# Optimization experiments

Measured on AMD Instinct MI355X. Metric: run time of the kernel, lower is better.

Reference implementation:

```python
import jax, jax.numpy as jnp
import numpy as np

B, H0, W0, C = 16, 56, 56, 96
NH, WS, SS = 3, 7, 3
HID, NCL, TAU = 384, 128, 0.5
EPS = 1e-6

def layernorm(x, g, b):
    m = jnp.mean(x, -1, keepdims=True)
    v = jnp.mean((x - m) ** 2, -1, keepdims=True)
    return (x - m) * jax.lax.rsqrt(v + 1e-5) * g + b

def setup_inputs() -> dict:
    key = jax.random.key(0)
    ks = jax.random.split(key, 16)
    s = lambda d: 1.0 / np.sqrt(d)
    return {
        "x": jax.random.normal(ks[0], (B, H0 * W0, C), jnp.float32),
        "norm1_g": jnp.ones((C,)), "norm1_b": jnp.zeros((C,)),
        "qkv_w": jax.random.normal(ks[1], (3 * C, C)) * s(C),
        "qkv_b": jnp.zeros((3 * C,)),
        "proj_w": jax.random.normal(ks[2], (C, C)) * s(C),
        "proj_b": jnp.zeros((C,)),
        "norm2_g": jnp.ones((C,)), "norm2_b": jnp.zeros((C,)),
        "ffn_norm_g": jnp.ones((C,)), "ffn_norm_b": jnp.zeros((C,)),
        "pin_w": jax.random.normal(ks[3], (HID, C)) * s(C),
        "pin_b": jnp.zeros((HID,)),
        "tm_inc": jax.random.normal(ks[4], (NCL, 2 * HID)) * 0.5,
        "tm_out": jax.random.normal(ks[5], (NCL, C)) * s(NCL),
        "gate": jnp.float32(0.5),
        "H": H0, "W": W0,
    }

def window_attention(win, qkv_w, qkv_b, proj_w, proj_b):
    N, T, Cc = win.shape
    hd = Cc // NH
    qkv = win @ qkv_w.T + qkv_b                      # [N, T, 3C]
    qkv = qkv.reshape(N, T, 3, NH, hd).transpose(2, 0, 3, 1, 4)
    q, k, v = qkv[0], qkv[1], qkv[2]                 # [N, nh, T, hd]
    attn = jax.nn.softmax(jnp.einsum('nhqd,nhkd->nhqk', q, k) * (hd ** -0.5), axis=-1)
    out = jnp.einsum('nhqk,nhkd->nhqd', attn, v).transpose(0, 2, 1, 3).reshape(N, T, Cc)
    return out @ proj_w.T + proj_b

def tm_ffn(x, ffn_norm_g, ffn_norm_b, pin_w, pin_b, tm_inc, tm_out, gate):
    # x: [B, T, C]
    Bb, T, Cc = x.shape
    y = jax.nn.sigmoid(layernorm(x, ffn_norm_g, ffn_norm_b) @ pin_w.T + pin_b)  # [B,T,HID]
    flat = y.reshape(Bb * T, HID)
    lits = jnp.clip(jnp.concatenate([flat, 1.0 - flat], axis=-1), EPS, 1.0)     # [N, 2*HID]
    m = jax.nn.sigmoid(tm_inc)
    hard = (m > TAU).astype(m.dtype)
    m_ste = m + jax.lax.stop_gradient(hard - m)      # binary via STE
    # binary mask -> conjunction prod_k l_k^{m_jk} = exp(log(l) @ m^T)
    clauses = jnp.exp(jnp.log(lits) @ m_ste.T)       # [N, NCL]
    logits = (clauses @ tm_out).reshape(Bb, T, Cc)
    g = jax.nn.sigmoid(gate)
    return g * logits + (1.0 - g) * jax.nn.sigmoid(logits)

def reference(x, norm1_g, norm1_b, qkv_w, qkv_b, proj_w, proj_b,
              norm2_g, norm2_b, ffn_norm_g, ffn_norm_b,
              pin_w, pin_b, tm_inc, tm_out, gate, H, W):
    Bb, L, Cc = x.shape
    shortcut = x
    y = layernorm(x, norm1_g, norm1_b).reshape(Bb, H, W, Cc)
    pad_h = (WS - H % WS) % WS
    pad_w = (WS - W % WS) % WS
    if pad_h or pad_w:
        y = jnp.pad(y, ((0, 0), (0, pad_h), (0, pad_w), (0, 0)))
    Hp, Wp = y.shape[1], y.shape[2]
    if SS > 0:
        y = jnp.roll(y, shift=(-SS, -SS), axis=(1, 2))
    # window partition
    y = y.reshape(Bb, Hp // WS, WS, Wp // WS, WS, Cc).transpose(0, 1, 3, 2, 4, 5)
    win = y.reshape(-1, WS * WS, Cc)
    a = window_attention(win, qkv_w, qkv_b, proj_w, proj_b)
    a = a.reshape(Bb, Hp // WS, Wp // WS, WS, WS, Cc)
    if SS > 0:
        a = jnp.roll(a, shift=(SS, SS), axis=(3, 4))
    # window reverse
    a = a.transpose(0, 1, 3, 2, 4, 5).reshape(Bb, Hp, Wp, Cc)
    if pad_h or pad_w:
        a = a[:, :H, :W, :]
    a = a.reshape(Bb, H * W, Cc)
    x1 = shortcut + a
    x2 = x1 + tm_ffn(layernorm(x1, norm2_g, norm2_b),
                     ffn_norm_g, ffn_norm_b, pin_w, pin_b, tm_inc, tm_out, gate)
    return x2
```

## Files before the change

### kernel.cpp

```cpp
#include <hip/hip_runtime.h>

#define NB 16
#define NHH 56
#define NWW 56
#define NC 96
#define NL (NHH*NWW)
#define NTOK (NB*NL)
#define WSZ 7
#define NT 49
#define SSH 3
#define NWIN 1024
#define HDIM 32
#define HID_ 384
#define NCL_ 128
#define NLIT 768
#define EPS_ 1e-6f

typedef unsigned short u16;
typedef unsigned int   u32;
typedef __attribute__((ext_vector_type(8))) short short8;
typedef __attribute__((ext_vector_type(4))) float f32x4;

__device__ __forceinline__ float us2f(u16 u) {
  union { u32 u; float f; } x; x.u = ((u32)u) << 16; return x.f;
}
__device__ __forceinline__ u16 f2us(float f) {
  union { float f; u32 u; } x; x.f = f;
  u32 lsb = (x.u >> 16) & 1u;
  return (u16)((x.u + 0x7fffu + lsb) >> 16);
}
__device__ __forceinline__ float sigmoidf_(float x) { return 1.f / (1.f + __expf(-x)); }

__global__ __launch_bounds__(256) void k0_prep(const float* __restrict__ tm_inc,
                                               const float* __restrict__ pin_w,
                                               const float* __restrict__ tm_out,
                                               const float* __restrict__ qkv_w,
                                               const float* __restrict__ proj_w,
                                               u16* __restrict__ maskb,
                                               u16* __restrict__ pinwb,
                                               u16* __restrict__ tmoT,
                                               u16* __restrict__ qkvwb,
                                               u16* __restrict__ projwb) {
  int idx = blockIdx.x * 256 + threadIdx.x;
  if (idx < NCL_ * NLIT)
    maskb[idx] = (tm_inc[idx] > 0.f) ? (u16)0x3F80 : (u16)0;
  if (idx < HID_ * NC)
    pinwb[idx] = f2us(pin_w[idx]);
  if (idx < NC * NCL_) {
    int c = idx / NCL_, k = idx - c * NCL_;
    tmoT[idx] = f2us(tm_out[(size_t)k * NC + c]);
  }
  if (idx < 3 * NC * NC)
    qkvwb[idx] = f2us(qkv_w[idx]);
  if (idx < NC * NC)
    projwb[idx] = f2us(proj_w[idx]);
}

__global__ __launch_bounds__(256) void k2_attn(const float* __restrict__ x,
                                               const float* __restrict__ n1g,
                                               const float* __restrict__ n1b,
                                               const u16* __restrict__ qkvwb,
                                               const float* __restrict__ qkv_b,
                                               const u16* __restrict__ projwb,
                                               const float* __restrict__ proj_b,
                                               float* __restrict__ x1) {
  __shared__ __align__(16) u16 syb[64 * 104];
  __shared__ __align__(16) u16 sq [64 * 104];
  __shared__ __align__(16) u16 sk [64 * 104];
  __shared__ __align__(16) u16 svT[96 * 72];
  __shared__ __align__(16) u16 sp [4 * 16 * 72];
  const int tid  = threadIdx.x;
  const int wave = tid >> 6;
  const int lane = tid & 63;
  const int l16  = lane & 15;
  const int quad = lane >> 4;
  const int win  = blockIdx.x;
  const int t0   = wave * 16;
  const int bb = win >> 6, wl = win & 63;
  const int hbase = (wl >> 3) * WSZ, wbase = (wl & 7) * WSZ;

  {
    const int t = tid >> 2, s = tid & 3;
    if (t < NT) {
      int hp = hbase + t / WSZ, wp = wbase + t % WSZ;
      int h = hp + SSH; if (h >= NHH) h -= NHH;
      int w = wp + SSH; if (w >= NWW) w -= NWW;
      const float* xp = x + ((size_t)bb * NL + (size_t)h * NWW + w) * NC;
      float4 v[6];
      float sum = 0.f;
      #pragma unroll
      for (int k = 0; k < 6; ++k) {
        v[k] = *reinterpret_cast<const float4*>(xp + s * 4 + k * 16);
        sum += v[k].x + v[k].y + v[k].z + v[k].w;
      }
      sum += __shfl_xor(sum, 1); sum += __shfl_xor(sum, 2);
      float mean = sum * (1.f / 96.f);
      float ssq = 0.f;
      #pragma unroll
      for (int k = 0; k < 6; ++k) {
        float d0 = v[k].x - mean, d1 = v[k].y - mean;
        float d2 = v[k].z - mean, d3 = v[k].w - mean;
        ssq += d0 * d0 + d1 * d1 + d2 * d2 + d3 * d3;
      }
      ssq += __shfl_xor(ssq, 1); ssq += __shfl_xor(ssq, 2);
      float rstd = rsqrtf(ssq * (1.f / 96.f) + 1e-5f);
      #pragma unroll
      for (int k = 0; k < 6; ++k) {
        int c = s * 4 + k * 16;
        const float4 g4 = *reinterpret_cast<const float4*>(n1g + c);
        const float4 b4 = *reinterpret_cast<const float4*>(n1b + c);
        syb[t * 104 + c + 0] = f2us((v[k].x - mean) * rstd * g4.x + b4.x);
        syb[t * 104 + c + 1] = f2us((v[k].y - mean) * rstd * g4.y + b4.y);
        syb[t * 104 + c + 2] = f2us((v[k].z - mean) * rstd * g4.z + b4.z);
        syb[t * 104 + c + 3] = f2us((v[k].w - mean) * rstd * g4.w + b4.w);
      }
    } else {
      #pragma unroll
      for (int k = 0; k < 6; ++k) {
        int c = s * 4 + k * 16;
        syb[t * 104 + c + 0] = 0; syb[t * 104 + c + 1] = 0;
        syb[t * 104 + c + 2] = 0; syb[t * 104 + c + 3] = 0;
      }
    }
  }
  __syncthreads();

  {
    short8 afr[3];
    #pragma unroll
    for (int ks = 0; ks < 3; ++ks)
      afr[ks] = *reinterpret_cast<const short8*>(&syb[(t0 + l16) * 104 + quad * 8 + ks * 32]);
    short8 rb[4][3];
    #pragma unroll
    for (int p = 0; p < 4; ++p)
      #pragma unroll
      for (int ks = 0; ks < 3; ++ks)
        rb[p][ks] = *reinterpret_cast<const short8*>(
            qkvwb + (size_t)(p * 16 + l16) * NC + quad * 8 + ks * 32);
    #pragma unroll
    for (int nt = 0; nt < 18; ++nt) {
      const int n0 = nt * 16;
      const float bias = qkv_b[n0 + l16];
      short8 b0 = rb[nt & 3][0], b1 = rb[nt & 3][1], b2 = rb[nt & 3][2];
      if (nt + 4 < 18) {
        #pragma unroll
        for (int ks = 0; ks < 3; ++ks)
          rb[nt & 3][ks] = *reinterpret_cast<const short8*>(
              qkvwb + (size_t)((nt + 4) * 16 + l16) * NC + quad * 8 + ks * 32);
      }
      f32x4 acc = {0.f, 0.f, 0.f, 0.f};
      acc = __builtin_amdgcn_mfma_f32_16x16x32_bf16(afr[0], b0, acc, 0, 0, 0);
      acc = __builtin_amdgcn_mfma_f32_16x16x32_bf16(afr[1], b1, acc, 0, 0, 0);
      acc = __builtin_amdgcn_mfma_f32_16x16x32_bf16(afr[2], b2, acc, 0, 0, 0);
      const int part = nt / 6;
      const int oc = n0 - part * 96 + l16;
      if (part < 2) {
        u16* dst = (part == 0) ? sq : sk;
        #pragma unroll
        for (int r = 0; r < 4; ++r)
          dst[(t0 + quad * 4 + r) * 104 + oc] = f2us(acc[r] + bias);
      } else {
        #pragma unroll
        for (int r = 0; r < 4; ++r)
          svT[oc * 72 + (t0 + quad * 4 + r)] = f2us(acc[r] + bias);
      }
    }
  }
  __syncthreads();

  u16* spw = sp + wave * 16 * 72;
  const float sscale = 0.17677669529663687f;
  for (int h = 0; h < 3; ++h) {
    const int d0 = h * HDIM;
    short8 qf = *reinterpret_cast<const short8*>(&sq[(t0 + l16) * 104 + d0 + quad * 8]);
    f32x4 s[4];
    #pragma unroll
    for (int nt = 0; nt < 4; ++nt) {
      short8 kf = *reinterpret_cast<const short8*>(&sk[(nt * 16 + l16) * 104 + d0 + quad * 8]);
      f32x4 a = {0.f, 0.f, 0.f, 0.f};
      s[nt] = __builtin_amdgcn_mfma_f32_16x16x32_bf16(qf, kf, a, 0, 0, 0);
    }
    #pragma unroll
    for (int nt = 0; nt < 4; ++nt)
      #pragma unroll
      for (int r = 0; r < 4; ++r) s[nt][r] *= sscale;
    if (l16 >= 1) {
      #pragma unroll
      for (int r = 0; r < 4; ++r) s[3][r] = -1e30f;
    }
    #pragma unroll
    for (int r = 0; r < 4; ++r) {
      float m = fmaxf(fmaxf(s[0][r], s[1][r]), fmaxf(s[2][r], s[3][r]));
      #pragma unroll
      for (int off = 8; off > 0; off >>= 1) m = fmaxf(m, __shfl_xor(m, off, 16));
      float e0 = __expf(s[0][r] - m), e1 = __expf(s[1][r] - m);
      float e2 = __expf(s[2][r] - m), e3 = __expf(s[3][r] - m);
      float sum = e0 + e1 + e2 + e3;
      #pragma unroll
      for (int off = 8; off > 0; off >>= 1) sum += __shfl_xor(sum, off, 16);
      float inv = 1.f / sum;
      const int row = quad * 4 + r;
      spw[row * 72 +      l16] = f2us(e0 * inv);
      spw[row * 72 + 16 + l16] = f2us(e1 * inv);
      spw[row * 72 + 32 + l16] = f2us(e2 * inv);
      spw[row * 72 + 48 + l16] = f2us(e3 * inv);
    }
    short8 pa[2];
    pa[0] = *reinterpret_cast<const short8*>(&spw[l16 * 72 + quad * 8]);
    pa[1] = *reinterpret_cast<const short8*>(&spw[l16 * 72 + 32 + quad * 8]);
    #pragma unroll
    for (int nt = 0; nt < 2; ++nt) {
      const int c0 = d0 + nt * 16;
      f32x4 acc = {0.f, 0.f, 0.f, 0.f};
      #pragma unroll
      for (int ks = 0; ks < 2; ++ks) {
        short8 vb = *reinterpret_cast<const short8*>(&svT[(c0 + l16) * 72 + ks * 32 + quad * 8]);
        acc = __builtin_amdgcn_mfma_f32_16x16x32_bf16(pa[ks], vb, acc, 0, 0, 0);
      }
      #pragma unroll
      for (int r = 0; r < 4; ++r)
        syb[(t0 + quad * 4 + r) * 104 + c0 + l16] = f2us(acc[r]);
    }
  }

  {
    short8 aa[3];
    #pragma unroll
    for (int ks = 0; ks < 3; ++ks)
      aa[ks] = *reinterpret_cast<const short8*>(&syb[(t0 + l16) * 104 + quad * 8 + ks * 32]);

    size_t tokr[4]; bool tval[4];
    #pragma unroll
    for (int r = 0; r < 4; ++r) {
      const int t = t0 + quad * 4 + r;
      tval[r] = (t < NT);
      int rr = t / WSZ + SSH; if (rr >= WSZ) rr -= WSZ;
      int qq = t % WSZ + SSH; if (qq >= WSZ) qq -= WSZ;
      tokr[r] = (size_t)bb * NL + (size_t)(hbase + rr) * NWW + (wbase + qq);
    }
    float xv[6][4];
    #pragma unroll
    for (int nt = 0; nt < 6; ++nt)
      #pragma unroll
      for (int r = 0; r < 4; ++r)
        xv[nt][r] = tval[r] ? x[tokr[r] * NC + nt * 16 + l16] : 0.f;

    short8 pbr[2][3];
    #pragma unroll
    for (int ks = 0; ks < 3; ++ks)
      pbr[0][ks] = *reinterpret_cast<const short8*>(
          projwb + (size_t)l16 * NC + quad * 8 + ks * 32);
    #pragma unroll
    for (int nt = 0; nt < 6; ++nt) {
      const int n0 = nt * 16;
      const float pb = proj_b[n0 + l16];
      short8 b0 = pbr[nt & 1][0], b1 = pbr[nt & 1][1], b2 = pbr[nt & 1][2];
      if (nt + 1 < 6) {
        #pragma unroll
        for (int ks = 0; ks < 3; ++ks)
          pbr[(nt + 1) & 1][ks] = *reinterpret_cast<const short8*>(
              projwb + (size_t)((nt + 1) * 16 + l16) * NC + quad * 8 + ks * 32);
      }
      f32x4 acc = {0.f, 0.f, 0.f, 0.f};
      acc = __builtin_amdgcn_mfma_f32_16x16x32_bf16(aa[0], b0, acc, 0, 0, 0);
      acc = __builtin_amdgcn_mfma_f32_16x16x32_bf16(aa[1], b1, acc, 0, 0, 0);
      acc = __builtin_amdgcn_mfma_f32_16x16x32_bf16(aa[2], b2, acc, 0, 0, 0);
      #pragma unroll
      for (int r = 0; r < 4; ++r) {
        if (tval[r])
          x1[tokr[r] * NC + n0 + l16] = xv[nt][r] + acc[r] + pb;
      }
    }
  }
}

__global__ __launch_bounds__(512) void k4_ffn(const float* __restrict__ x1,
                                              const float* __restrict__ g2,
                                              const float* __restrict__ b2,
                                              const float* __restrict__ gf,
                                              const float* __restrict__ bf,
                                              const u16* __restrict__ pinwb,
                                              const float* __restrict__ pin_b,
                                              const u16* __restrict__ maskb,
                                              const u16* __restrict__ tmoT,
                                              const float* __restrict__ gate,
                                              float* __restrict__ out) {
  __shared__ __align__(16) u16 szb[32 * 104];
  __shared__ __align__(16) u16 lit[32 * 776];
  __shared__ __align__(16) u16 claT[32 * 136];
  __shared__ __align__(16) float sx1[32 * 100];
  const int tid  = threadIdx.x;
  const int wave = tid >> 6;
  const int lane = tid & 63;
  const int l16  = lane & 15;
  const int quad = lane >> 4;
  const size_t tok0 = (size_t)blockIdx.x * 32;

  {
    const int t = tid >> 4, s = tid & 15;
    const float* xp = x1 + (tok0 + t) * NC;
    float2 v[3];
    float sum = 0.f;
    #pragma unroll
    for (int k = 0; k < 3; ++k) {
      const int c = s * 2 + k * 32;
      v[k] = *reinterpret_cast<const float2*>(xp + c);
      sum += v[k].x + v[k].y;
      *reinterpret_cast<float2*>(&sx1[t * 100 + c]) = v[k];
    }
    #pragma unroll
    for (int off = 8; off > 0; off >>= 1) sum += __shfl_xor(sum, off, 16);
    const float mean = sum * (1.f / 96.f);
    float ssq = 0.f;
    #pragma unroll
    for (int k = 0; k < 3; ++k) {
      float d0 = v[k].x - mean, d1 = v[k].y - mean;
      ssq += d0 * d0 + d1 * d1;
    }
    #pragma unroll
    for (int off = 8; off > 0; off >>= 1) ssq += __shfl_xor(ssq, off, 16);
    const float rstd = rsqrtf(ssq * (1.f / 96.f) + 1e-5f);
    float tv[6];
    float sum2 = 0.f;
    #pragma unroll
    for (int k = 0; k < 3; ++k) {
      const int c = s * 2 + k * 32;
      const float2 gg = *reinterpret_cast<const float2*>(g2 + c);
      const float2 bb = *reinterpret_cast<const float2*>(b2 + c);
      tv[2 * k]     = (v[k].x - mean) * rstd * gg.x + bb.x;
      tv[2 * k + 1] = (v[k].y - mean) * rstd * gg.y + bb.y;
      sum2 += tv[2 * k] + tv[2 * k + 1];
    }
    #pragma unroll
    for (int off = 8; off > 0; off >>= 1) sum2 += __shfl_xor(sum2, off, 16);
    const float mean2 = sum2 * (1.f / 96.f);
    float ssq2 = 0.f;
    #pragma unroll
    for (int k = 0; k < 3; ++k) {
      float d0 = tv[2 * k] - mean2, d1 = tv[2 * k + 1] - mean2;
      ssq2 += d0 * d0 + d1 * d1;
    }
    #pragma unroll
    for (int off = 8; off > 0; off >>= 1) ssq2 += __shfl_xor(ssq2, off, 16);
    const float rstd2 = rsqrtf(ssq2 * (1.f / 96.f) + 1e-5f);
    #pragma unroll
    for (int k = 0; k < 3; ++k) {
      const int c = s * 2 + k * 32;
      const float2 gg = *reinterpret_cast<const float2*>(gf + c);
      const float2 bb = *reinterpret_cast<const float2*>(bf + c);
      u16 lo = f2us((tv[2 * k]     - mean2) * rstd2 * gg.x + bb.x);
      u16 hi = f2us((tv[2 * k + 1] - mean2) * rstd2 * gg.y + bb.y);
      *reinterpret_cast<u32*>(&szb[t * 104 + c]) = (u32)lo | ((u32)hi << 16);
    }
  }
  __syncthreads();

  const float gv = sigmoidf_(gate[0]);

  short8 a_pin[2][3];
  #pragma unroll
  for (int mt = 0; mt < 2; ++mt)
    #pragma unroll
    for (int ks = 0; ks < 3; ++ks)
      a_pin[mt][ks] = *reinterpret_cast<const short8*>(
          &szb[(mt * 16 + l16) * 104 + quad * 8 + ks * 32]);

  {
    float pbias[3];
    #pragma unroll
    for (int i = 0; i < 3; ++i) pbias[i] = pin_b[(wave * 3 + i) * 16 + l16];
    short8 pb[2][3];
    #pragma unroll
    for (int ks = 0; ks < 3; ++ks)
      pb[0][ks] = *reinterpret_cast<const short8*>(
          pinwb + (size_t)(wave * 3 * 16 + l16) * NC + quad * 8 + ks * 32);
    #pragma unroll
    for (int i = 0; i < 3; ++i) {
      short8 b0 = pb[i & 1][0], b1 = pb[i & 1][1], b2 = pb[i & 1][2];
      if (i + 1 < 3) {
        const int n1 = (wave * 3 + i + 1) * 16;
        #pragma unroll
        for (int ks = 0; ks < 3; ++ks)
          pb[(i + 1) & 1][ks] = *reinterpret_cast<const short8*>(
              pinwb + (size_t)(n1 + l16) * NC + quad * 8 + ks * 32);
      }
      f32x4 acc0 = {0.f, 0.f, 0.f, 0.f}, acc1 = {0.f, 0.f, 0.f, 0.f};
      acc0 = __builtin_amdgcn_mfma_f32_16x16x32_bf16(a_pin[0][0], b0, acc0, 0, 0, 0);
      acc1 = __builtin_amdgcn_mfma_f32_16x16x32_bf16(a_pin[1][0], b0, acc1, 0, 0, 0);
      acc0 = __builtin_amdgcn_mfma_f32_16x16x32_bf16(a_pin[0][1], b1, acc0, 0, 0, 0);
      acc1 = __builtin_amdgcn_mfma_f32_16x16x32_bf16(a_pin[1][1], b1, acc1, 0, 0, 0);
      acc0 = __builtin_amdgcn_mfma_f32_16x16x32_bf16(a_pin[0][2], b2, acc0, 0, 0, 0);
      acc1 = __builtin_amdgcn_mfma_f32_16x16x32_bf16(a_pin[1][2], b2, acc1, 0, 0, 0);
      const int o = (wave * 3 + i) * 16 + l16;
      const float pbv = pbias[i];
      #pragma unroll
      for (int r = 0; r < 4; ++r) {
        float y0 = sigmoidf_(acc0[r] + pbv);
        float y1 = sigmoidf_(acc1[r] + pbv);
        const int ta = quad * 4 + r, tb = 16 + quad * 4 + r;
        lit[ta * 776 + o]       = f2us(__logf(fmaxf(y0, EPS_)));
        lit[ta * 776 + 384 + o] = f2us(__logf(fmaxf(1.f - y0, EPS_)));
        lit[tb * 776 + o]       = f2us(__logf(fmaxf(y1, EPS_)));
        lit[tb * 776 + 384 + o] = f2us(__logf(fmaxf(1.f - y1, EPS_)));
      }
    }
  }
  __syncthreads();

  {
    const int ct = wave;
    const u16* bp0 = maskb + (size_t)(ct * 16 + l16) * NLIT + quad * 8;
    short8 rb0[4];
    #pragma unroll
    for (int p = 0; p < 4; ++p)
      rb0[p] = *reinterpret_cast<const short8*>(bp0 + p * 32);
    f32x4 c00 = {0.f, 0.f, 0.f, 0.f}, c10 = {0.f, 0.f, 0.f, 0.f};
    #pragma unroll
    for (int ks = 0; ks < 24; ++ks) {
      const int k0 = ks * 32 + quad * 8;
      short8 a0 = *reinterpret_cast<const short8*>(&lit[l16 * 776 + k0]);
      short8 a1 = *reinterpret_cast<const short8*>(&lit[(16 + l16) * 776 + k0]);
      short8 b0 = rb0[ks & 3];
      if (ks + 4 < 24)
        rb0[ks & 3] = *reinterpret_cast<const short8*>(bp0 + (ks + 4) * 32);
      c00 = __builtin_amdgcn_mfma_f32_16x16x32_bf16(a0, b0, c00, 0, 0, 0);
      c10 = __builtin_amdgcn_mfma_f32_16x16x32_bf16(a1, b0, c10, 0, 0, 0);
    }
    #pragma unroll
    for (int r = 0; r < 4; ++r) {
      const int ta = quad * 4 + r, tb = 16 + quad * 4 + r;
      claT[ta * 136 + ct * 16 + l16] = f2us(__expf(c00[r]));
      claT[tb * 136 + ct * 16 + l16] = f2us(__expf(c10[r]));
    }
  }
  __syncthreads();

  if (wave < 6) {
    const int nt = wave;
    f32x4 acc0 = {0.f, 0.f, 0.f, 0.f}, acc1 = {0.f, 0.f, 0.f, 0.f};
    #pragma unroll
    for (int ks = 0; ks < 4; ++ks) {
      const int k0 = ks * 32 + quad * 8;
      short8 a0 = *reinterpret_cast<const short8*>(&claT[l16 * 136 + k0]);
      short8 a1 = *reinterpret_cast<const short8*>(&claT[(16 + l16) * 136 + k0]);
      short8 b = *reinterpret_cast<const short8*>(
          tmoT + (size_t)(nt * 16 + l16) * NCL_ + k0);
      acc0 = __builtin_amdgcn_mfma_f32_16x16x32_bf16(a0, b, acc0, 0, 0, 0);
      acc1 = __builtin_amdgcn_mfma_f32_16x16x32_bf16(a1, b, acc1, 0, 0, 0);
    }
    const int c = nt * 16 + l16;
    #pragma unroll
    for (int r = 0; r < 4; ++r) {
      const int ta = quad * 4 + r, tb = 16 + quad * 4 + r;
      float lg0 = acc0[r], lg1 = acc1[r];
      out[(tok0 + ta) * NC + c] = sx1[ta * 100 + c] + gv * lg0 + (1.f - gv) * sigmoidf_(lg0);
      out[(tok0 + tb) * NC + c] = sx1[tb * 100 + c] + gv * lg1 + (1.f - gv) * sigmoidf_(lg1);
    }
  }
}

extern "C" void kernel_launch(void* const* d_in, const int* in_sizes, int n_in,
                              void* d_out, int out_size, void* d_ws, size_t ws_size,
                              hipStream_t stream) {
  (void)in_sizes; (void)n_in; (void)out_size; (void)ws_size;
  const float* x      = (const float*)d_in[0];
  const float* n1g    = (const float*)d_in[1];
  const float* n1b    = (const float*)d_in[2];
  const float* qkv_w  = (const float*)d_in[3];
  const float* qkv_b  = (const float*)d_in[4];
  const float* proj_w = (const float*)d_in[5];
  const float* proj_b = (const float*)d_in[6];
  const float* n2g    = (const float*)d_in[7];
  const float* n2b    = (const float*)d_in[8];
  const float* fng    = (const float*)d_in[9];
  const float* fnb    = (const float*)d_in[10];
  const float* pin_w  = (const float*)d_in[11];
  const float* pin_b  = (const float*)d_in[12];
  const float* tm_inc = (const float*)d_in[13];
  const float* tm_out = (const float*)d_in[14];
  const float* gate   = (const float*)d_in[15];

  float* x1 = (float*)d_ws;
  u16* maskb = (u16*)(x1 + (size_t)NTOK * NC);
  u16* pinwb = maskb + NCL_ * NLIT;
  u16* tmoT  = pinwb + HID_ * NC;
  u16* qkvwb = tmoT + NC * NCL_;
  u16* projwb= qkvwb + 3 * NC * NC;

  hipLaunchKernelGGL(k0_prep, dim3(384), dim3(256), 0, stream,
                     tm_inc, pin_w, tm_out, qkv_w, proj_w, maskb, pinwb, tmoT, qkvwb, projwb);
  hipLaunchKernelGGL(k2_attn, dim3(NWIN), dim3(256), 0, stream,
                     x, n1g, n1b, qkvwb, qkv_b, projwb, proj_b, x1);
  hipLaunchKernelGGL(k4_ffn, dim3(NTOK / 32), dim3(512), 0, stream,
                     x1, n2g, n2b, fng, fnb, pinwb, pin_b, maskb, tmoT, gate, (float*)d_out);
}
```

Before: 202.0 us.

## Split FFN clause stage into two token passes to shrink LDS footprint

```diff
diff --git a/kernel.cpp b/kernel.cpp
--- a/kernel.cpp
+++ b/kernel.cpp
@@ -15,6 +15,7 @@
 #define NCL_ 128
 #define NLIT 768
 #define EPS_ 1e-6f
+#define LOG_EPS -13.815510558f
 
 typedef unsigned short u16;
 typedef unsigned int   u32;
@@ -285,10 +286,10 @@
                                               const u16* __restrict__ tmoT,
                                               const float* __restrict__ gate,
                                               float* __restrict__ out) {
-  __shared__ __align__(16) u16 szb[32 * 104];
-  __shared__ __align__(16) u16 lit[32 * 776];
-  __shared__ __align__(16) u16 claT[32 * 136];
-  __shared__ __align__(16) float sx1[32 * 100];
+  __shared__ __align__(16) u16 lit[16 * 776];
+  __shared__ __align__(16) u16 su[32 * 136];
+  u16* szb  = su;
+  u16* claT = su;
   const int tid  = threadIdx.x;
   const int wave = tid >> 6;
   const int lane = tid & 63;
@@ -306,7 +307,6 @@
       const int c = s * 2 + k * 32;
       v[k] = *reinterpret_cast<const float2*>(xp + c);
       sum += v[k].x + v[k].y;
-      *reinterpret_cast<float2*>(&sx1[t * 100 + c]) = v[k];
     }
     #pragma unroll
     for (int off = 8; off > 0; off >>= 1) sum += __shfl_xor(sum, off, 16);
@@ -365,75 +365,71 @@
       a_pin[mt][ks] = *reinterpret_cast<const short8*>(
           &szb[(mt * 16 + l16) * 104 + quad * 8 + ks * 32]);
 
-  {
-    float pbias[3];
-    #pragma unroll
-    for (int i = 0; i < 3; ++i) pbias[i] = pin_b[(wave * 3 + i) * 16 + l16];
-    short8 pb[2][3];
-    #pragma unroll
-    for (int ks = 0; ks < 3; ++ks)
-      pb[0][ks] = *reinterpret_cast<const short8*>(
-          pinwb + (size_t)(wave * 3 * 16 + l16) * NC + quad * 8 + ks * 32);
-    #pragma unroll
-    for (int i = 0; i < 3; ++i) {
-      short8 b0 = pb[i & 1][0], b1 = pb[i & 1][1], b2 = pb[i & 1][2];
-      if (i + 1 < 3) {
-        const int n1 = (wave * 3 + i + 1) * 16;
+  float pbias[3];
+  #pragma unroll
+  for (int i = 0; i < 3; ++i) pbias[i] = pin_b[(wave * 3 + i) * 16 + l16];
+
+  #pragma unroll
+  for (int pass = 0; pass < 2; ++pass) {
+    {
+      short8 pb[2][3];
+      #pragma unroll
+      for (int ks = 0; ks < 3; ++ks)
+        pb[0][ks] = *reinterpret_cast<const short8*>(
+            pinwb + (size_t)(wave * 3 * 16 + l16) * NC + quad * 8 + ks * 32);
+      #pragma unroll
+      for (int i = 0; i < 3; ++i) {
+        short8 b0 = pb[i & 1][0], b1 = pb[i & 1][1], b2 = pb[i & 1][2];
+        if (i + 1 < 3) {
+          const int n1 = (wave * 3 + i + 1) * 16;
+          #pragma unroll
+          for (int ks = 0; ks < 3; ++ks)
+            pb[(i + 1) & 1][ks] = *reinterpret_cast<const short8*>(
+                pinwb + (size_t)(n1 + l16) * NC + quad * 8 + ks * 32);
+        }
+        f32x4 acc = {0.f, 0.f, 0.f, 0.f};
+        acc = __builtin_amdgcn_mfma_f32_16x16x32_bf16(a_pin[pass][0], b0, acc, 0, 0, 0);
+        acc = __builtin_amdgcn_mfma_f32_16x16x32_bf16(a_pin[pass][1], b1, acc, 0, 0, 0);
+        acc = __builtin_amdgcn_mfma_f32_16x16x32_bf16(a_pin[pass][2], b2, acc, 0, 0, 0);
+        const int o = (wave * 3 + i) * 16 + l16;
+        const float pbv = pbias[i];
         #pragma unroll
-        for (int ks = 0; ks < 3; ++ks)
-          pb[(i + 1) & 1][ks] = *reinterpret_cast<const short8*>(
-              pinwb + (size_t)(n1 + l16) * NC + quad * 8 + ks * 32);
-      }
-      f32x4 acc0 = {0.f, 0.f, 0.f, 0.f}, acc1 = {0.f, 0.f, 0.f, 0.f};
-      acc0 = __builtin_amdgcn_mfma_f32_16x16x32_bf16(a_pin[0][0], b0, acc0, 0, 0, 0);
-      acc1 = __builtin_amdgcn_mfma_f32_16x16x32_bf16(a_pin[1][0], b0, acc1, 0, 0, 0);
-      acc0 = __builtin_amdgcn_mfma_f32_16x16x32_bf16(a_pin[0][1], b1, acc0, 0, 0, 0);
-      acc1 = __builtin_amdgcn_mfma_f32_16x16x32_bf16(a_pin[1][1], b1, acc1, 0, 0, 0);
-      acc0 = __builtin_amdgcn_mfma_f32_16x16x32_bf16(a_pin[0][2], b2, acc0, 0, 0, 0);
-      acc1 = __builtin_amdgcn_mfma_f32_16x16x32_bf16(a_pin[1][2], b2, acc1, 0, 0, 0);
-      const int o = (wave * 3 + i) * 16 + l16;
-      const float pbv = pbias[i];
+        for (int r = 0; r < 4; ++r) {
+          const float a = acc[r] + pbv;
+          const float sp = fmaxf(a, 0.f) + __logf(1.f + __expf(-fabsf(a)));
+          const int t = quad * 4 + r;
+          lit[t * 776 + o]       = f2us(fmaxf(a - sp, LOG_EPS));
+          lit[t * 776 + 384 + o] = f2us(fmaxf(-sp, LOG_EPS));
+        }
+      }
+    }
+    __syncthreads();
+
+    {
+      const int ct = wave;
+      const u16* bp0 = maskb + (size_t)(ct * 16 + l16) * NLIT + quad * 8;
+      short8 rb0[4];
+      #pragma unroll
+      for (int p = 0; p < 4; ++p)
+        rb0[p] = *reinterpret_cast<const short8*>(bp0 + p * 32);
+      f32x4 c00 = {0.f, 0.f, 0.f, 0.f};
+      #pragma unroll
+      for (int ks = 0; ks < 24; ++ks) {
+        const int k0 = ks * 32 + quad * 8;
+        short8 a0 = *reinterpret_cast<const short8*>(&lit[l16 * 776 + k0]);
+        short8 b0 = rb0[ks & 3];
+        if (ks + 4 < 24)
+          rb0[ks & 3] = *reinterpret_cast<const short8*>(bp0 + (ks + 4) * 32);
+        c00 = __builtin_amdgcn_mfma_f32_16x16x32_bf16(a0, b0, c00, 0, 0, 0);
+      }
       #pragma unroll
       for (int r = 0; r < 4; ++r) {
-        float y0 = sigmoidf_(acc0[r] + pbv);
-        float y1 = sigmoidf_(acc1[r] + pbv);
-        const int ta = quad * 4 + r, tb = 16 + quad * 4 + r;
-        lit[ta * 776 + o]       = f2us(__logf(fmaxf(y0, EPS_)));
-        lit[ta * 776 + 384 + o] = f2us(__logf(fmaxf(1.f - y0, EPS_)));
-        lit[tb * 776 + o]       = f2us(__logf(fmaxf(y1, EPS_)));
-        lit[tb * 776 + 384 + o] = f2us(__logf(fmaxf(1.f - y1, EPS_)));
-      }
-    }
-  }
-  __syncthreads();
-
-  {
-    const int ct = wave;
-    const u16* bp0 = maskb + (size_t)(ct * 16 + l16) * NLIT + quad * 8;
-    short8 rb0[4];
-    #pragma unroll
-    for (int p = 0; p < 4; ++p)
-      rb0[p] = *reinterpret_cast<const short8*>(bp0 + p * 32);
-    f32x4 c00 = {0.f, 0.f, 0.f, 0.f}, c10 = {0.f, 0.f, 0.f, 0.f};
-    #pragma unroll
-    for (int ks = 0; ks < 24; ++ks) {
-      const int k0 = ks * 32 + quad * 8;
-      short8 a0 = *reinterpret_cast<const short8*>(&lit[l16 * 776 + k0]);
-      short8 a1 = *reinterpret_cast<const short8*>(&lit[(16 + l16) * 776 + k0]);
-      short8 b0 = rb0[ks & 3];
-      if (ks + 4 < 24)
-        rb0[ks & 3] = *reinterpret_cast<const short8*>(bp0 + (ks + 4) * 32);
-      c00 = __builtin_amdgcn_mfma_f32_16x16x32_bf16(a0, b0, c00, 0, 0, 0);
-      c10 = __builtin_amdgcn_mfma_f32_16x16x32_bf16(a1, b0, c10, 0, 0, 0);
-    }
-    #pragma unroll
-    for (int r = 0; r < 4; ++r) {
-      const int ta = quad * 4 + r, tb = 16 + quad * 4 + r;
-      claT[ta * 136 + ct * 16 + l16] = f2us(__expf(c00[r]));
-      claT[tb * 136 + ct * 16 + l16] = f2us(__expf(c10[r]));
-    }
-  }
-  __syncthreads();
+        const int t = pass * 16 + quad * 4 + r;
+        claT[t * 136 + ct * 16 + l16] = f2us(__expf(c00[r]));
+      }
+    }
+    __syncthreads();
+  }
 
   if (wave < 6) {
     const int nt = wave;
@@ -453,8 +449,10 @@
     for (int r = 0; r < 4; ++r) {
       const int ta = quad * 4 + r, tb = 16 + quad * 4 + r;
       float lg0 = acc0[r], lg1 = acc1[r];
-      out[(tok0 + ta) * NC + c] = sx1[ta * 100 + c] + gv * lg0 + (1.f - gv) * sigmoidf_(lg0);
-      out[(tok0 + tb) * NC + c] = sx1[tb * 100 + c] + gv * lg1 + (1.f - gv) * sigmoidf_(lg1);
+      out[(tok0 + ta) * NC + c] =
+          x1[(tok0 + ta) * NC + c] + gv * lg0 + (1.f - gv) * sigmoidf_(lg0);
+      out[(tok0 + tb) * NC + c] =
+          x1[(tok0 + tb) * NC + c] + gv * lg1 + (1.f - gv) * sigmoidf_(lg1);
     }
   }
 }
```

New measurement: 235.9 us. 1.17x slower.

## Interleave literal layout, compute log-sigmoid directly, and shrink FFN shared memory

Applied to the files above, without the earlier changes.

```diff
diff --git a/kernel.cpp b/kernel.cpp
--- a/kernel.cpp
+++ b/kernel.cpp
@@ -15,6 +15,7 @@
 #define NCL_ 128
 #define NLIT 768
 #define EPS_ 1e-6f
+#define LOG_EPS -13.815510558f
 
 typedef unsigned short u16;
 typedef unsigned int   u32;
@@ -42,8 +43,12 @@
                                                u16* __restrict__ qkvwb,
                                                u16* __restrict__ projwb) {
   int idx = blockIdx.x * 256 + threadIdx.x;
-  if (idx < NCL_ * NLIT)
-    maskb[idx] = (tm_inc[idx] > 0.f) ? (u16)0x3F80 : (u16)0;
+  if (idx < NCL_ * NLIT) {
+    int k = idx / NLIT, j = idx - k * NLIT;
+    int o   = (j < HID_) ? j : (j - HID_);
+    int pos = (j < HID_) ? (2 * o) : (2 * o + 1);
+    maskb[(size_t)k * NLIT + pos] = (tm_inc[idx] > 0.f) ? (u16)0x3F80 : (u16)0;
+  }
   if (idx < HID_ * NC)
     pinwb[idx] = f2us(pin_w[idx]);
   if (idx < NC * NCL_) {
@@ -285,10 +290,10 @@
                                               const u16* __restrict__ tmoT,
                                               const float* __restrict__ gate,
                                               float* __restrict__ out) {
-  __shared__ __align__(16) u16 szb[32 * 104];
-  __shared__ __align__(16) u16 lit[32 * 776];
-  __shared__ __align__(16) u16 claT[32 * 136];
-  __shared__ __align__(16) float sx1[32 * 100];
+  __shared__ __align__(16) u16 lit[32 * 778];
+  __shared__ __align__(16) u16 su[32 * 140];
+  u16* szb  = su;
+  u16* claT = su;
   const int tid  = threadIdx.x;
   const int wave = tid >> 6;
   const int lane = tid & 63;
@@ -306,7 +311,6 @@
       const int c = s * 2 + k * 32;
       v[k] = *reinterpret_cast<const float2*>(xp + c);
       sum += v[k].x + v[k].y;
-      *reinterpret_cast<float2*>(&sx1[t * 100 + c]) = v[k];
     }
     #pragma unroll
     for (int off = 8; off > 0; off >>= 1) sum += __shfl_xor(sum, off, 16);
@@ -391,17 +395,21 @@
       acc1 = __builtin_amdgcn_mfma_f32_16x16x32_bf16(a_pin[1][1], b1, acc1, 0, 0, 0);
       acc0 = __builtin_amdgcn_mfma_f32_16x16x32_bf16(a_pin[0][2], b2, acc0, 0, 0, 0);
       acc1 = __builtin_amdgcn_mfma_f32_16x16x32_bf16(a_pin[1][2], b2, acc1, 0, 0, 0);
-      const int o = (wave * 3 + i) * 16 + l16;
+      const int o2 = ((wave * 3 + i) * 16 + l16) * 2;
       const float pbv = pbias[i];
       #pragma unroll
       for (int r = 0; r < 4; ++r) {
-        float y0 = sigmoidf_(acc0[r] + pbv);
-        float y1 = sigmoidf_(acc1[r] + pbv);
+        const float a0 = acc0[r] + pbv;
+        const float sp0 = fmaxf(a0, 0.f) + __logf(1.f + __expf(-fabsf(a0)));
+        const u16 la0 = f2us(fmaxf(a0 - sp0, LOG_EPS));
+        const u16 lb0 = f2us(fmaxf(-sp0, LOG_EPS));
+        const float a1 = acc1[r] + pbv;
+        const float sp1 = fmaxf(a1, 0.f) + __logf(1.f + __expf(-fabsf(a1)));
+        const u16 la1 = f2us(fmaxf(a1 - sp1, LOG_EPS));
+        const u16 lb1 = f2us(fmaxf(-sp1, LOG_EPS));
         const int ta = quad * 4 + r, tb = 16 + quad * 4 + r;
-        lit[ta * 776 + o]       = f2us(__logf(fmaxf(y0, EPS_)));
-        lit[ta * 776 + 384 + o] = f2us(__logf(fmaxf(1.f - y0, EPS_)));
-        lit[tb * 776 + o]       = f2us(__logf(fmaxf(y1, EPS_)));
-        lit[tb * 776 + 384 + o] = f2us(__logf(fmaxf(1.f - y1, EPS_)));
+        *reinterpret_cast<u32*>(&lit[ta * 778 + o2]) = (u32)la0 | ((u32)lb0 << 16);
+        *reinterpret_cast<u32*>(&lit[tb * 778 + o2]) = (u32)la1 | ((u32)lb1 << 16);
       }
     }
   }
@@ -418,8 +426,8 @@
     #pragma unroll
     for (int ks = 0; ks < 24; ++ks) {
       const int k0 = ks * 32 + quad * 8;
-      short8 a0 = *reinterpret_cast<const short8*>(&lit[l16 * 776 + k0]);
-      short8 a1 = *reinterpret_cast<const short8*>(&lit[(16 + l16) * 776 + k0]);
+      short8 a0 = *reinterpret_cast<const short8*>(&lit[l16 * 778 + k0]);
+      short8 a1 = *reinterpret_cast<const short8*>(&lit[(16 + l16) * 778 + k0]);
       short8 b0 = rb0[ks & 3];
       if (ks + 4 < 24)
         rb0[ks & 3] = *reinterpret_cast<const short8*>(bp0 + (ks + 4) * 32);
@@ -429,8 +437,8 @@
     #pragma unroll
     for (int r = 0; r < 4; ++r) {
       const int ta = quad * 4 + r, tb = 16 + quad * 4 + r;
-      claT[ta * 136 + ct * 16 + l16] = f2us(__expf(c00[r]));
-      claT[tb * 136 + ct * 16 + l16] = f2us(__expf(c10[r]));
+      claT[ta * 140 + ct * 16 + l16] = f2us(__expf(c00[r]));
+      claT[tb * 140 + ct * 16 + l16] = f2us(__expf(c10[r]));
     }
   }
   __syncthreads();
@@ -441,8 +449,8 @@
     #pragma unroll
     for (int ks = 0; ks < 4; ++ks) {
       const int k0 = ks * 32 + quad * 8;
-      short8 a0 = *reinterpret_cast<const short8*>(&claT[l16 * 136 + k0]);
-      short8 a1 = *reinterpret_cast<const short8*>(&claT[(16 + l16) * 136 + k0]);
+      short8 a0 = *reinterpret_cast<const short8*>(&claT[l16 * 140 + k0]);
+      short8 a1 = *reinterpret_cast<const short8*>(&claT[(16 + l16) * 140 + k0]);
       short8 b = *reinterpret_cast<const short8*>(
           tmoT + (size_t)(nt * 16 + l16) * NCL_ + k0);
       acc0 = __builtin_amdgcn_mfma_f32_16x16x32_bf16(a0, b, acc0, 0, 0, 0);
@@ -453,8 +461,10 @@
     for (int r = 0; r < 4; ++r) {
       const int ta = quad * 4 + r, tb = 16 + quad * 4 + r;
       float lg0 = acc0[r], lg1 = acc1[r];
-      out[(tok0 + ta) * NC + c] = sx1[ta * 100 + c] + gv * lg0 + (1.f - gv) * sigmoidf_(lg0);
-      out[(tok0 + tb) * NC + c] = sx1[tb * 100 + c] + gv * lg1 + (1.f - gv) * sigmoidf_(lg1);
+      out[(tok0 + ta) * NC + c] =
+          x1[(tok0 + ta) * NC + c] + gv * lg0 + (1.f - gv) * sigmoidf_(lg0);
+      out[(tok0 + tb) * NC + c] =
+          x1[(tok0 + tb) * NC + c] + gv * lg1 + (1.f - gv) * sigmoidf_(lg1);
     }
   }
 }
```

After: 204.8 us. No clear change (+1.4%).

## Shrink FFN kernel LDS by aliasing buffers and computing log-sigmoid directly

Applied to the files above, without the earlier changes.

```diff
diff --git a/kernel.cpp b/kernel.cpp
--- a/kernel.cpp
+++ b/kernel.cpp
@@ -15,6 +15,7 @@
 #define NCL_ 128
 #define NLIT 768
 #define EPS_ 1e-6f
+#define LOG_EPS -13.815510558f
 
 typedef unsigned short u16;
 typedef unsigned int   u32;
@@ -285,10 +286,10 @@
                                               const u16* __restrict__ tmoT,
                                               const float* __restrict__ gate,
                                               float* __restrict__ out) {
-  __shared__ __align__(16) u16 szb[32 * 104];
   __shared__ __align__(16) u16 lit[32 * 776];
-  __shared__ __align__(16) u16 claT[32 * 136];
-  __shared__ __align__(16) float sx1[32 * 100];
+  __shared__ __align__(16) u16 su[32 * 136];
+  u16* szb  = su;
+  u16* claT = su;
   const int tid  = threadIdx.x;
   const int wave = tid >> 6;
   const int lane = tid & 63;
@@ -306,7 +307,6 @@
       const int c = s * 2 + k * 32;
       v[k] = *reinterpret_cast<const float2*>(xp + c);
       sum += v[k].x + v[k].y;
-      *reinterpret_cast<float2*>(&sx1[t * 100 + c]) = v[k];
     }
     #pragma unroll
     for (int off = 8; off > 0; off >>= 1) sum += __shfl_xor(sum, off, 16);
@@ -369,50 +369,56 @@
     float pbias[3];
     #pragma unroll
     for (int i = 0; i < 3; ++i) pbias[i] = pin_b[(wave * 3 + i) * 16 + l16];
-    short8 pb[2][3];
-    #pragma unroll
-    for (int ks = 0; ks < 3; ++ks)
-      pb[0][ks] = *reinterpret_cast<const short8*>(
-          pinwb + (size_t)(wave * 3 * 16 + l16) * NC + quad * 8 + ks * 32);
+    short8 pb[3][3];
+    #pragma unroll
+    for (int i = 0; i < 3; ++i)
+      #pragma unroll
+      for (int ks = 0; ks < 3; ++ks)
+        pb[i][ks] = *reinterpret_cast<const short8*>(
+            pinwb + (size_t)((wave * 3 + i) * 16 + l16) * NC + quad * 8 + ks * 32);
     #pragma unroll
     for (int i = 0; i < 3; ++i) {
-      short8 b0 = pb[i & 1][0], b1 = pb[i & 1][1], b2 = pb[i & 1][2];
-      if (i + 1 < 3) {
-        const int n1 = (wave * 3 + i + 1) * 16;
-        #pragma unroll
-        for (int ks = 0; ks < 3; ++ks)
-          pb[(i + 1) & 1][ks] = *reinterpret_cast<const short8*>(
-              pinwb + (size_t)(n1 + l16) * NC + quad * 8 + ks * 32);
-      }
       f32x4 acc0 = {0.f, 0.f, 0.f, 0.f}, acc1 = {0.f, 0.f, 0.f, 0.f};
-      acc0 = __builtin_amdgcn_mfma_f32_16x16x32_bf16(a_pin[0][0], b0, acc0, 0, 0, 0);
-      acc1 = __builtin_amdgcn_mfma_f32_16x16x32_bf16(a_pin[1][0], b0, acc1, 0, 0, 0);
-      acc0 = __builtin_amdgcn_mfma_f32_16x16x32_bf16(a_pin[0][1], b1, acc0, 0, 0, 0);
-      acc1 = __builtin_amdgcn_mfma_f32_16x16x32_bf16(a_pin[1][1], b1, acc1, 0, 0, 0);
-      acc0 = __builtin_amdgcn_mfma_f32_16x16x32_bf16(a_pin[0][2], b2, acc0, 0, 0, 0);
-      acc1 = __builtin_amdgcn_mfma_f32_16x16x32_bf16(a_pin[1][2], b2, acc1, 0, 0, 0);
+      acc0 = __builtin_amdgcn_mfma_f32_16x16x32_bf16(a_pin[0][0], pb[i][0], acc0, 0, 0, 0);
+      acc1 = __builtin_amdgcn_mfma_f32_16x16x32_bf16(a_pin[1][0], pb[i][0], acc1, 0, 0, 0);
+      acc0 = __builtin_amdgcn_mfma_f32_16x16x32_bf16(a_pin[0][1], pb[i][1], acc0, 0, 0, 0);
+      acc1 = __builtin_amdgcn_mfma_f32_16x16x32_bf16(a_pin[1][1], pb[i][1], acc1, 0, 0, 0);
+      acc0 = __builtin_amdgcn_mfma_f32_16x16x32_bf16(a_pin[0][2], pb[i][2], acc0, 0, 0, 0);
+      acc1 = __builtin_amdgcn_mfma_f32_16x16x32_bf16(a_pin[1][2], pb[i][2], acc1, 0, 0, 0);
       const int o = (wave * 3 + i) * 16 + l16;
       const float pbv = pbias[i];
       #pragma unroll
       for (int r = 0; r < 4; ++r) {
-        float y0 = sigmoidf_(acc0[r] + pbv);
-        float y1 = sigmoidf_(acc1[r] + pbv);
+        const float a0 = acc0[r] + pbv;
+        const float sp0 = fmaxf(a0, 0.f) + __logf(1.f + __expf(-fabsf(a0)));
+        const float a1 = acc1[r] + pbv;
+        const float sp1 = fmaxf(a1, 0.f) + __logf(1.f + __expf(-fabsf(a1)));
         const int ta = quad * 4 + r, tb = 16 + quad * 4 + r;
-        lit[ta * 776 + o]       = f2us(__logf(fmaxf(y0, EPS_)));
-        lit[ta * 776 + 384 + o] = f2us(__logf(fmaxf(1.f - y0, EPS_)));
-        lit[tb * 776 + o]       = f2us(__logf(fmaxf(y1, EPS_)));
-        lit[tb * 776 + 384 + o] = f2us(__logf(fmaxf(1.f - y1, EPS_)));
+        lit[ta * 776 + o]       = f2us(fmaxf(a0 - sp0, LOG_EPS));
+        lit[ta * 776 + 384 + o] = f2us(fmaxf(-sp0, LOG_EPS));
+        lit[tb * 776 + o]       = f2us(fmaxf(a1 - sp1, LOG_EPS));
+        lit[tb * 776 + 384 + o] = f2us(fmaxf(-sp1, LOG_EPS));
       }
     }
   }
   __syncthreads();
+
+  float xr[2][4];
+  if (wave < 6) {
+    const int c = wave * 16 + l16;
+    #pragma unroll
+    for (int r = 0; r < 4; ++r) {
+      xr[0][r] = x1[(tok0 + quad * 4 + r) * NC + c];
+      xr[1][r] = x1[(tok0 + 16 + quad * 4 + r) * NC + c];
+    }
+  }
 
   {
     const int ct = wave;
     const u16* bp0 = maskb + (size_t)(ct * 16 + l16) * NLIT + quad * 8;
-    short8 rb0[4];
-    #pragma unroll
-    for (int p = 0; p < 4; ++p)
+    short8 rb0[8];
+    #pragma unroll
+    for (int p = 0; p < 8; ++p)
       rb0[p] = *reinterpret_cast<const short8*>(bp0 + p * 32);
     f32x4 c00 = {0.f, 0.f, 0.f, 0.f}, c10 = {0.f, 0.f, 0.f, 0.f};
     #pragma unroll
@@ -420,9 +426,9 @@
       const int k0 = ks * 32 + quad * 8;
       short8 a0 = *reinterpret_cast<const short8*>(&lit[l16 * 776 + k0]);
       short8 a1 = *reinterpret_cast<const short8*>(&lit[(16 + l16) * 776 + k0]);
-      short8 b0 = rb0[ks & 3];
-      if (ks + 4 < 24)
-        rb0[ks & 3] = *reinterpret_cast<const short8*>(bp0 + (ks + 4) * 32);
+      short8 b0 = rb0[ks & 7];
+      if (ks + 8 < 24)
+        rb0[ks & 7] = *reinterpret_cast<const short8*>(bp0 + (ks + 8) * 32);
       c00 = __builtin_amdgcn_mfma_f32_16x16x32_bf16(a0, b0, c00, 0, 0, 0);
       c10 = __builtin_amdgcn_mfma_f32_16x16x32_bf16(a1, b0, c10, 0, 0, 0);
     }
@@ -437,24 +443,27 @@
 
   if (wave < 6) {
     const int nt = wave;
+    short8 btm[4];
+    #pragma unroll
+    for (int ks = 0; ks < 4; ++ks)
+      btm[ks] = *reinterpret_cast<const short8*>(
+          tmoT + (size_t)(nt * 16 + l16) * NCL_ + ks * 32 + quad * 8);
     f32x4 acc0 = {0.f, 0.f, 0.f, 0.f}, acc1 = {0.f, 0.f, 0.f, 0.f};
     #pragma unroll
     for (int ks = 0; ks < 4; ++ks) {
       const int k0 = ks * 32 + quad * 8;
       short8 a0 = *reinterpret_cast<const short8*>(&claT[l16 * 136 + k0]);
       short8 a1 = *reinterpret_cast<const short8*>(&claT[(16 + l16) * 136 + k0]);
-      short8 b = *reinterpret_cast<const short8*>(
-          tmoT + (size_t)(nt * 16 + l16) * NCL_ + k0);
-      acc0 = __builtin_amdgcn_mfma_f32_16x16x32_bf16(a0, b, acc0, 0, 0, 0);
-      acc1 = __builtin_amdgcn_mfma_f32_16x16x32_bf16(a1, b, acc1, 0, 0, 0);
+      acc0 = __builtin_amdgcn_mfma_f32_16x16x32_bf16(a0, btm[ks], acc0, 0, 0, 0);
+      acc1 = __builtin_amdgcn_mfma_f32_16x16x32_bf16(a1, btm[ks], acc1, 0, 0, 0);
     }
     const int c = nt * 16 + l16;
     #pragma unroll
     for (int r = 0; r < 4; ++r) {
       const int ta = quad * 4 + r, tb = 16 + quad * 4 + r;
       float lg0 = acc0[r], lg1 = acc1[r];
-      out[(tok0 + ta) * NC + c] = sx1[ta * 100 + c] + gv * lg0 + (1.f - gv) * sigmoidf_(lg0);
-      out[(tok0 + tb) * NC + c] = sx1[tb * 100 + c] + gv * lg1 + (1.f - gv) * sigmoidf_(lg1);
+      out[(tok0 + ta) * NC + c] = xr[0][r] + gv * lg0 + (1.f - gv) * sigmoidf_(lg0);
+      out[(tok0 + tb) * NC + c] = xr[1][r] + gv * lg1 + (1.f - gv) * sigmoidf_(lg1);
     }
   }
 }
```

Measured after the change: 196.6 us. 2.7% less time.
